# Kernel optimization log

Measured on AMD Instinct MI355X. Metric: run time of the kernel, lower is better.

The kernel has to match this reference:

```python
import jax, jax.numpy as jnp
import numpy as np

B, NQ, NK, D_IN, D_H = 2, 8192, 8192, 256, 256


def setup_inputs() -> dict:
    key = jax.random.key(0)
    ks = jax.random.split(key, 9)
    s = 1.0 / np.sqrt(D_IN)
    return {
        "q": jax.random.normal(ks[0], (B, NQ, D_IN), jnp.float32),
        "k": jax.random.normal(ks[1], (B, NK, D_IN), jnp.float32),
        "v": jax.random.normal(ks[2], (B, NK, D_IN), jnp.float32),
        "Wq": jax.random.uniform(ks[3], (D_IN, D_H), jnp.float32, -s, s),
        "bq": jax.random.uniform(ks[4], (D_H,), jnp.float32, -s, s),
        "Wk": jax.random.uniform(ks[5], (D_IN, D_H), jnp.float32, -s, s),
        "bk": jax.random.uniform(ks[6], (D_H,), jnp.float32, -s, s),
        "Wv": jax.random.uniform(ks[7], (D_IN, D_H), jnp.float32, -s, s),
        "bv": jax.random.uniform(ks[8], (D_H,), jnp.float32, -s, s),
        "chunk_size": 1024,
    }


def reference(q, k, v, Wq, bq, Wk, bk, Wv, bv, chunk_size):
    # Projections (nn.Linear: x @ W + b)
    q_emb = q @ Wq + bq            # [B, NQ, D_H]
    k_emb = k @ Wk + bk            # [B, NK, D_H]
    v_emb = v @ Wv + bv            # value_emb=True -> project v
    # NOTE: original applies NO 1/sqrt(d) scaling.
    # Query chunking in the original is a pure memory optimization;
    # softmax is over the full key axis, so full attention is identical math.
    scores = jnp.einsum("bqd,bkd->bqk", q_emb, k_emb)  # [B, NQ, NK]
    probs = jax.nn.softmax(scores, axis=-1)
    out = jnp.einsum("bqk,bkd->bqd", probs, v_emb)     # [B, NQ, D_H]
    return out
```

## Files before the change

### kernel.cpp

```cpp
#include <hip/hip_runtime.h>

#define B_   2
#define NQ_  8192
#define NK_  8192
#define DIN_ 256
#define DH_  256
#define M_   (B_ * NQ_)

typedef _Float16 f16x8 __attribute__((ext_vector_type(8)));
typedef unsigned short u16x8 __attribute__((ext_vector_type(8)));
typedef unsigned short u16x4 __attribute__((ext_vector_type(4)));
typedef unsigned int  u32x4 __attribute__((ext_vector_type(4)));
typedef float f32x16 __attribute__((ext_vector_type(16)));

__device__ __forceinline__ unsigned short f2h(float f) {
    _Float16 h = (_Float16)f;
    return __builtin_bit_cast(unsigned short, h);
}
__device__ __forceinline__ float h2f(unsigned short u) {
    return (float)__builtin_bit_cast(_Float16, u);
}

__global__ void wt_conv(const float* __restrict__ Wq, const float* __restrict__ Wk,
                        const float* __restrict__ Wv, unsigned short* __restrict__ wpack) {
    __shared__ float tile[64][65];
    const int mat = blockIdx.z;
    const int k0 = blockIdx.x * 64, n0 = blockIdx.y * 64;
    const float* W = (mat == 0) ? Wq : (mat == 1) ? Wk : Wv;
#pragma unroll
    for (int p = 0; p < 16; ++p) {
        const int idx = p * 256 + threadIdx.x;
        const int r = idx >> 6, c = idx & 63;
        tile[r][c] = W[(k0 + r) * 256 + n0 + c];
    }
    __syncthreads();
    unsigned short* wp = wpack + mat * 65536;
#pragma unroll
    for (int p = 0; p < 2; ++p) {
        const int e = p * 256 + threadIdx.x;
        const int kk8 = e >> 6;
        const int nn = e & 63;
        const int ks = (k0 >> 4) + (kk8 >> 1);
        const int lh = kk8 & 1;
        const int ng = (n0 >> 5) + (nn >> 5);
        const int l = (nn & 31) + 32 * lh;
        u16x8 val;
#pragma unroll
        for (int j = 0; j < 8; ++j) val[j] = f2h(tile[kk8 * 8 + j][nn]);
        *(u16x8*)(wp + ((size_t)(ks * 8 + ng) * 64 + l) * 8) = val;
    }
}

__global__ __launch_bounds__(256) void proj(
    const float* __restrict__ xq, const float* __restrict__ xk, const float* __restrict__ xv,
    const float* __restrict__ bq, const float* __restrict__ bk, const float* __restrict__ bv,
    const unsigned short* __restrict__ wpack,
    unsigned short* __restrict__ q_emb, unsigned short* __restrict__ k_emb,
    unsigned short* __restrict__ vpack) {
    __shared__ __align__(16) unsigned short xt[64 * 256];
    const int mat = blockIdx.y;
    const float* x    = (mat == 0) ? xq : (mat == 1) ? xk : xv;
    const float* bias = (mat == 0) ? bq : (mat == 1) ? bk : bv;
    const unsigned short* wp = wpack + mat * 65536;

    const int tid = threadIdx.x;
    const int l = tid & 63, wv = tid >> 6;
    const int pair = wv >> 1, h = wv & 1;
    const int lm = l & 31, lh = l >> 5;
    const int row0 = blockIdx.x * 64;

    {
        const float* xb = x + (size_t)row0 * 256;
#pragma unroll
        for (int p = 0; p < 8; ++p) {
            const int idx = p * 256 + tid;
            const int r = idx >> 5;
            const int c8 = idx & 31;
            const float4* ap = (const float4*)(xb + r * 256 + c8 * 8);
            float4 a0 = ap[0], a1 = ap[1];
            u16x8 au;
            au[0] = f2h(a0.x); au[1] = f2h(a0.y); au[2] = f2h(a0.z); au[3] = f2h(a0.w);
            au[4] = f2h(a1.x); au[5] = f2h(a1.y); au[6] = f2h(a1.z); au[7] = f2h(a1.w);
            *(u16x8*)(xt + r * 256 + (c8 ^ (r & 31)) * 8) = au;
        }
    }
    __syncthreads();

    f32x16 acc[4];
#pragma unroll
    for (int i = 0; i < 4; ++i)
#pragma unroll
        for (int j = 0; j < 16; ++j) acc[i][j] = 0.0f;

#pragma unroll
    for (int ks = 0; ks < 16; ++ks) {
        f16x8 af = *(const f16x8*)(xt + (pair * 32 + lm) * 256 +
                                   (((ks * 2 + lh) ^ lm) * 8));
#pragma unroll
        for (int nt = 0; nt < 4; ++nt) {
            f16x8 bfr = *(const f16x8*)(wp + ((size_t)(ks * 8 + h * 4 + nt) * 64 + l) * 8);
            acc[nt] = __builtin_amdgcn_mfma_f32_32x32x16_f16(af, bfr, acc[nt], 0, 0, 0);
        }
    }

    if (mat < 2) {
        unsigned short* emb = (mat == 0) ? q_emb : k_emb;
#pragma unroll
        for (int nt = 0; nt < 4; ++nt) {
            const int n = h * 128 + nt * 32 + lm;
            const float bsv = bias[n];
#pragma unroll
            for (int r = 0; r < 16; ++r) {
                const int rl = (r & 3) + 8 * (r >> 2) + 4 * lh;
                emb[(size_t)(row0 + pair * 32 + rl) * 256 + n] = f2h(acc[nt][r] + bsv);
            }
        }
    } else {
        const int batch = row0 >> 13;
        const int m0 = (row0 & 8191) + pair * 32;
        unsigned short* vp = vpack + (size_t)batch * (512 * 8 * 64 * 8);
        const int base_kt = m0 >> 4;
#pragma unroll
        for (int nt = 0; nt < 4; ++nt) {
            const int dg = h * 4 + nt;
            const int n = h * 128 + nt * 32 + lm;
            const float bsv = bias[n];
#pragma unroll
            for (int g = 0; g < 4; ++g) {
                u16x4 pk;
#pragma unroll
                for (int i = 0; i < 4; ++i) pk[i] = f2h(acc[nt][4 * g + i] + bsv);
                const int kt = base_kt + (g >> 1);
                const int lane = (g & 1) * 32 + lm;
                *(u16x4*)(vp + ((size_t)(kt * 8 + dg) * 64 + lane) * 8 + lh * 4) = pk;
            }
        }
    }
}

#define BN_ 128
#define NT_ (NK_ / BN_)
#define KB_BYTES 65536
#define PSTRIDE 272
#define PBYTES  (64 * PSTRIDE)
#define STAT_OFF (2 * KB_BYTES + PBYTES)
#define LDS_TOTAL (STAT_OFF + 2048)

__global__ __launch_bounds__(512, 2) void flash(
    const unsigned short* __restrict__ q_emb, const unsigned short* __restrict__ k_emb,
    const unsigned short* __restrict__ vpack, float* __restrict__ out) {
    __shared__ __align__(16) char lds_raw[LDS_TOTAL];
    char* pbuf = lds_raw + 2 * KB_BYTES;
    float* smax = (float*)(lds_raw + STAT_OFF);
    float* ssum = smax + 256;
    float* alph = ssum + 256;
    float* linvb = alph + 64;

    const int tid = threadIdx.x;
    const int l = tid & 63, wv = tid >> 6;
    const int kq = wv >> 1, pair = wv & 1;
    const int lm = l & 31, lh = l >> 5;

    const int bx = blockIdx.x;
    const int batch = bx >> 7;
    const int qb = (bx & 127) * 64;

    const unsigned short* kg = k_emb + (size_t)batch * NK_ * 256;
    const unsigned short* vp = vpack + (size_t)batch * (512 * 8 * 64 * 8);

    const int mrow = batch * NQ_ + qb + pair * 32 + lm;
    f16x8 qf[16];
#pragma unroll
    for (int ks = 0; ks < 16; ++ks)
        qf[ks] = *(const f16x8*)(q_emb + (size_t)mrow * 256 + ks * 16 + lh * 8);

    f32x16 oacc[2];
#pragma unroll
    for (int i = 0; i < 2; ++i)
#pragma unroll
        for (int j = 0; j < 16; ++j) oacc[i][j] = 0.0f;

    float mstat = -3.0e38f, lstat = 0.0f;

    const int rlane = l >> 5;
    const int gl = l & 31;
    auto stage_k = [&](int kb, char* kdst) {
#pragma unroll
        for (int p = 0; p < 8; ++p) {
            const int r0 = wv * 16 + 2 * p;
            const int r = r0 + rlane;
            const int gsw = gl ^ (r & 31);
            const unsigned short* src = kg + (size_t)(kb + r) * 256 + gsw * 8;
            __builtin_amdgcn_global_load_lds(
                (const __attribute__((address_space(1))) void*)src,
                (__attribute__((address_space(3))) void*)(kdst + r0 * 512),
                16, 0, 0);
        }
    };

    f16x8 vf[8];
    auto load_v = [&](int kb) {
        const size_t kt0 = (size_t)(kb >> 4);
#pragma unroll
        for (int ks2 = 0; ks2 < 8; ++ks2)
            vf[ks2] = *(const f16x8*)(vp + (((kt0 + ks2) * 8 + wv) * 64 + l) * 8);
    };

    stage_k(0, lds_raw);
    __syncthreads();

    const int prow = pair * 32 + lm;

    for (int t = 0; t < NT_; ++t) {
        const int kb = t * BN_;
        char* kcur = lds_raw + (t & 1) * KB_BYTES;
        if (t + 1 < NT_) stage_k(kb + BN_, lds_raw + ((t + 1) & 1) * KB_BYTES);
        load_v(kb);

        f32x16 s;
#pragma unroll
        for (int j = 0; j < 16; ++j) s[j] = 0.0f;
#pragma unroll
        for (int ks = 0; ks < 16; ++ks) {
            const int gsw = (2 * ks + lh) ^ lm;
            f16x8 kf = *(const f16x8*)(kcur + (kq * 32 + lm) * 512 + gsw * 16);
            s = __builtin_amdgcn_mfma_f32_32x32x16_f16(kf, qf[ks], s, 0, 0, 0);
        }

        float pm = s[0];
#pragma unroll
        for (int j = 1; j < 16; ++j) pm = fmaxf(pm, s[j]);
        pm = fmaxf(pm, __shfl_xor(pm, 32, 64));
        if (lh == 0) smax[prow * 4 + kq] = pm;
        __syncthreads();

        const float4 m4 = *(const float4*)&smax[prow * 4];
        const float gm = fmaxf(fmaxf(m4.x, m4.y), fmaxf(m4.z, m4.w));
        const float mn = fmaxf(mstat, gm);
        const float alpha = __expf(mstat - mn);
        mstat = mn;
        if (kq == 0 && lh == 0) alph[prow] = alpha;

        float psum = 0.0f;
#pragma unroll
        for (int g = 0; g < 4; ++g) {
            u16x4 pk;
#pragma unroll
            for (int j = 0; j < 4; ++j) {
                const unsigned short hh = f2h(__expf(s[g * 4 + j] - mn));
                pk[j] = hh;
                psum += h2f(hh);
            }
            *(u16x4*)(pbuf + prow * PSTRIDE + (kq * 32 + 8 * g + 4 * lh) * 2) = pk;
        }
        psum += __shfl_xor(psum, 32, 64);
        if (lh == 0) ssum[prow * 4 + kq] = psum;
        __syncthreads();

        const float4 s4 = *(const float4*)&ssum[prow * 4];
        lstat = lstat * alpha + (s4.x + s4.y) + (s4.z + s4.w);

        const float a0 = alph[lm];
        const float a1 = alph[lm + 32];
#pragma unroll
        for (int j = 0; j < 16; ++j) oacc[0][j] *= a0;
#pragma unroll
        for (int j = 0; j < 16; ++j) oacc[1][j] *= a1;

#pragma unroll
        for (int ks2 = 0; ks2 < 8; ++ks2) {
            const f16x8 vfr = vf[ks2];
            f16x8 pf0 = *(const f16x8*)(pbuf + lm * PSTRIDE + ks2 * 32 + lh * 16);
            f16x8 pf1 = *(const f16x8*)(pbuf + (lm + 32) * PSTRIDE + ks2 * 32 + lh * 16);
            oacc[0] = __builtin_amdgcn_mfma_f32_32x32x16_f16(vfr, pf0, oacc[0], 0, 0, 0);
            oacc[1] = __builtin_amdgcn_mfma_f32_32x32x16_f16(vfr, pf1, oacc[1], 0, 0, 0);
        }
    }

    if (kq == 0 && lh == 0) linvb[prow] = 1.0f / lstat;
    __syncthreads();
    const float linv0 = linvb[lm];
    const float linv1 = linvb[lm + 32];
#pragma unroll
    for (int qt = 0; qt < 2; ++qt) {
        const float lv = qt ? linv1 : linv0;
        float* orow = out + (size_t)(batch * NQ_ + qb + qt * 32 + lm) * 256 + wv * 32;
#pragma unroll
        for (int g = 0; g < 4; ++g) {
            float4 o4;
            o4.x = oacc[qt][4 * g + 0] * lv;
            o4.y = oacc[qt][4 * g + 1] * lv;
            o4.z = oacc[qt][4 * g + 2] * lv;
            o4.w = oacc[qt][4 * g + 3] * lv;
            *(float4*)(orow + 8 * g + 4 * lh) = o4;
        }
    }
}

extern "C" void kernel_launch(void* const* d_in, const int* in_sizes, int n_in,
                              void* d_out, int out_size, void* d_ws, size_t ws_size,
                              hipStream_t stream) {
    const float* q  = (const float*)d_in[0];
    const float* k  = (const float*)d_in[1];
    const float* v  = (const float*)d_in[2];
    const float* Wq = (const float*)d_in[3];
    const float* bq = (const float*)d_in[4];
    const float* Wk = (const float*)d_in[5];
    const float* bk = (const float*)d_in[6];
    const float* Wv = (const float*)d_in[7];
    const float* bv = (const float*)d_in[8];
    float* out = (float*)d_out;

    unsigned short* wpack   = (unsigned short*)d_ws;
    unsigned short* q_emb   = wpack + 3 * 65536;
    unsigned short* k_emb   = q_emb + (size_t)M_ * DH_;
    unsigned short* vpack   = k_emb + (size_t)M_ * DH_;

    wt_conv<<<dim3(4, 4, 3), 256, 0, stream>>>(Wq, Wk, Wv, wpack);
    proj<<<dim3(256, 3), 256, 0, stream>>>(q, k, v, bq, bk, bv, wpack, q_emb, k_emb, vpack);
    flash<<<256, 512, 0, stream>>>(q_emb, k_emb, vpack, out);
}
```

Before: 286.3 us.

## Split flash attention into specialized QK/softmax and PV warps with pipelined tiles

Restructures the flash kernel so that two waves compute QK^T scores and softmax while two other waves run the PV accumulation one tile behind, using double-buffered P, max and sum arrays in LDS. The key tile drops from 128 to 64, the query block from 64 to 32 rows, and the launch becomes 512 blocks of 256 threads. The goal is to overlap the softmax and QK MFMA work with the PV MFMA work and to let each PV wave reuse one P fragment across four output tiles. The cost is less MFMA parallelism per block, since only half the waves do each phase. Each K tile is also reloaded for only 32 queries, which doubles K traffic, and PV waves hold 64 accumulator registers plus 16 V fragments each.

```diff
diff --git a/kernel.cpp b/kernel.cpp
--- a/kernel.cpp
+++ b/kernel.cpp
@@ -138,49 +138,36 @@
     }
 }
 
-#define BN_ 128
-#define NT_ (NK_ / BN_)
-#define KB_BYTES 65536
-#define PSTRIDE 272
-#define PBYTES  (64 * PSTRIDE)
-#define STAT_OFF (2 * KB_BYTES + PBYTES)
-#define LDS_TOTAL (STAT_OFF + 2048)
-
-__global__ __launch_bounds__(512, 2) void flash(
+#define BN6_ 64
+#define NT6_ (NK_ / BN6_)
+#define KTILE_B 32768
+#define PST6 144
+#define PBUF_OFF (2 * KTILE_B)
+#define SMAX_OFF (PBUF_OFF + 2 * 32 * PST6)
+#define SSUM_OFF (SMAX_OFF + 512)
+#define LDS6_TOTAL (SSUM_OFF + 512)
+
+__global__ __launch_bounds__(256, 2) void flash(
     const unsigned short* __restrict__ q_emb, const unsigned short* __restrict__ k_emb,
     const unsigned short* __restrict__ vpack, float* __restrict__ out) {
-    __shared__ __align__(16) char lds_raw[LDS_TOTAL];
-    char* pbuf = lds_raw + 2 * KB_BYTES;
-    float* smax = (float*)(lds_raw + STAT_OFF);
-    float* ssum = smax + 256;
-    float* alph = ssum + 256;
-    float* linvb = alph + 64;
+    __shared__ __align__(16) char lds_raw[LDS6_TOTAL];
+    char* pb = lds_raw + PBUF_OFF;
+    float* smax = (float*)(lds_raw + SMAX_OFF);
+    float* ssum = (float*)(lds_raw + SSUM_OFF);
 
     const int tid = threadIdx.x;
     const int l = tid & 63, wv = tid >> 6;
-    const int kq = wv >> 1, pair = wv & 1;
     const int lm = l & 31, lh = l >> 5;
+    const bool is_s = (wv < 2);
+    const int kq = wv & 1;
+    const int pw = wv & 1;
 
     const int bx = blockIdx.x;
-    const int batch = bx >> 7;
-    const int qb = (bx & 127) * 64;
+    const int batch = bx >> 8;
+    const int qb = (bx & 255) * 32;
 
     const unsigned short* kg = k_emb + (size_t)batch * NK_ * 256;
     const unsigned short* vp = vpack + (size_t)batch * (512 * 8 * 64 * 8);
-
-    const int mrow = batch * NQ_ + qb + pair * 32 + lm;
-    f16x8 qf[16];
-#pragma unroll
-    for (int ks = 0; ks < 16; ++ks)
-        qf[ks] = *(const f16x8*)(q_emb + (size_t)mrow * 256 + ks * 16 + lh * 8);
-
-    f32x16 oacc[2];
-#pragma unroll
-    for (int i = 0; i < 2; ++i)
-#pragma unroll
-        for (int j = 0; j < 16; ++j) oacc[i][j] = 0.0f;
-
-    float mstat = -3.0e38f, lstat = 0.0f;
 
     const int rlane = l >> 5;
     const int gl = l & 31;
@@ -198,101 +185,147 @@
         }
     };
 
-    f16x8 vf[8];
-    auto load_v = [&](int kb) {
-        const size_t kt0 = (size_t)(kb >> 4);
-#pragma unroll
-        for (int ks2 = 0; ks2 < 8; ++ks2)
-            vf[ks2] = *(const f16x8*)(vp + (((kt0 + ks2) * 8 + wv) * 64 + l) * 8);
-    };
+    f16x8 qf[16];
+    float mstat_s = -3.0e38f;
+    f16x8 vf[16];
+    f32x16 oacc[4];
+    float mstat_p = -3.0e38f, lstat = 0.0f;
+
+    if (is_s) {
+        const int mrow = batch * NQ_ + qb + lm;
+#pragma unroll
+        for (int ks = 0; ks < 16; ++ks)
+            qf[ks] = *(const f16x8*)(q_emb + (size_t)mrow * 256 + ks * 16 + lh * 8);
+    } else {
+#pragma unroll
+        for (int i = 0; i < 4; ++i)
+#pragma unroll
+            for (int j = 0; j < 16; ++j) oacc[i][j] = 0.0f;
+    }
 
     stage_k(0, lds_raw);
     __syncthreads();
 
-    const int prow = pair * 32 + lm;
-
-    for (int t = 0; t < NT_; ++t) {
-        const int kb = t * BN_;
-        char* kcur = lds_raw + (t & 1) * KB_BYTES;
-        if (t + 1 < NT_) stage_k(kb + BN_, lds_raw + ((t + 1) & 1) * KB_BYTES);
-        load_v(kb);
+    for (int t = 0; t < NT6_; ++t) {
+        const int kb = t * BN6_;
+        if (t + 1 < NT6_) stage_k(kb + BN6_, lds_raw + ((t + 1) & 1) * KTILE_B);
 
         f32x16 s;
-#pragma unroll
-        for (int j = 0; j < 16; ++j) s[j] = 0.0f;
-#pragma unroll
-        for (int ks = 0; ks < 16; ++ks) {
-            const int gsw = (2 * ks + lh) ^ lm;
-            f16x8 kf = *(const f16x8*)(kcur + (kq * 32 + lm) * 512 + gsw * 16);
-            s = __builtin_amdgcn_mfma_f32_32x32x16_f16(kf, qf[ks], s, 0, 0, 0);
-        }
-
-        float pm = s[0];
-#pragma unroll
-        for (int j = 1; j < 16; ++j) pm = fmaxf(pm, s[j]);
-        pm = fmaxf(pm, __shfl_xor(pm, 32, 64));
-        if (lh == 0) smax[prow * 4 + kq] = pm;
+        if (is_s) {
+            char* kcur = lds_raw + (t & 1) * KTILE_B;
+#pragma unroll
+            for (int j = 0; j < 16; ++j) s[j] = 0.0f;
+#pragma unroll
+            for (int ks = 0; ks < 16; ++ks) {
+                const int gsw = (2 * ks + lh) ^ lm;
+                f16x8 kf = *(const f16x8*)(kcur + (kq * 32 + lm) * 512 + gsw * 16);
+                s = __builtin_amdgcn_mfma_f32_32x32x16_f16(kf, qf[ks], s, 0, 0, 0);
+            }
+            float pm = s[0];
+#pragma unroll
+            for (int j = 1; j < 16; ++j) pm = fmaxf(pm, s[j]);
+            pm = fmaxf(pm, __shfl_xor(pm, 32, 64));
+            if (lh == 0) smax[(t & 1) * 64 + lm * 2 + kq] = pm;
+        } else {
+            if (t > 0) {
+                const int pp = (t - 1) & 1;
+                const float m0 = smax[pp * 64 + lm * 2 + 0];
+                const float m1 = smax[pp * 64 + lm * 2 + 1];
+                const float gm = fmaxf(m0, m1);
+                const float mn = fmaxf(mstat_p, gm);
+                const float alpha = __expf(mstat_p - mn);
+                mstat_p = mn;
+                const float s0 = ssum[pp * 64 + lm * 2 + 0];
+                const float s1 = ssum[pp * 64 + lm * 2 + 1];
+                lstat = lstat * alpha + (s0 + s1);
+#pragma unroll
+                for (int dgi = 0; dgi < 4; ++dgi)
+#pragma unroll
+                    for (int j = 0; j < 16; ++j) oacc[dgi][j] *= alpha;
+                char* pbr = pb + pp * 32 * PST6;
+#pragma unroll
+                for (int ks2 = 0; ks2 < 4; ++ks2) {
+                    f16x8 pf = *(const f16x8*)(pbr + lm * PST6 + ks2 * 32 + lh * 16);
+#pragma unroll
+                    for (int dgi = 0; dgi < 4; ++dgi)
+                        oacc[dgi] = __builtin_amdgcn_mfma_f32_32x32x16_f16(
+                            vf[ks2 * 4 + dgi], pf, oacc[dgi], 0, 0, 0);
+                }
+            }
+            const size_t kt0 = (size_t)(kb >> 4);
+#pragma unroll
+            for (int ks2 = 0; ks2 < 4; ++ks2)
+#pragma unroll
+                for (int dgi = 0; dgi < 4; ++dgi)
+                    vf[ks2 * 4 + dgi] = *(const f16x8*)(
+                        vp + (((kt0 + ks2) * 8 + pw * 4 + dgi) * 64 + l) * 8);
+        }
         __syncthreads();
 
-        const float4 m4 = *(const float4*)&smax[prow * 4];
-        const float gm = fmaxf(fmaxf(m4.x, m4.y), fmaxf(m4.z, m4.w));
-        const float mn = fmaxf(mstat, gm);
-        const float alpha = __expf(mstat - mn);
-        mstat = mn;
-        if (kq == 0 && lh == 0) alph[prow] = alpha;
-
-        float psum = 0.0f;
-#pragma unroll
-        for (int g = 0; g < 4; ++g) {
-            u16x4 pk;
-#pragma unroll
-            for (int j = 0; j < 4; ++j) {
-                const unsigned short hh = f2h(__expf(s[g * 4 + j] - mn));
-                pk[j] = hh;
-                psum += h2f(hh);
-            }
-            *(u16x4*)(pbuf + prow * PSTRIDE + (kq * 32 + 8 * g + 4 * lh) * 2) = pk;
-        }
-        psum += __shfl_xor(psum, 32, 64);
-        if (lh == 0) ssum[prow * 4 + kq] = psum;
+        if (is_s) {
+            const float m0 = smax[(t & 1) * 64 + lm * 2 + 0];
+            const float m1 = smax[(t & 1) * 64 + lm * 2 + 1];
+            const float gm = fmaxf(m0, m1);
+            const float mn = fmaxf(mstat_s, gm);
+            mstat_s = mn;
+            char* pbw = pb + (t & 1) * 32 * PST6;
+            float psum = 0.0f;
+#pragma unroll
+            for (int g = 0; g < 4; ++g) {
+                u16x4 pk;
+#pragma unroll
+                for (int j = 0; j < 4; ++j) {
+                    const unsigned short hh = f2h(__expf(s[g * 4 + j] - mn));
+                    pk[j] = hh;
+                    psum += h2f(hh);
+                }
+                *(u16x4*)(pbw + lm * PST6 + kq * 64 + 16 * g + 8 * lh) = pk;
+            }
+            psum += __shfl_xor(psum, 32, 64);
+            if (lh == 0) ssum[(t & 1) * 64 + lm * 2 + kq] = psum;
+        }
         __syncthreads();
-
-        const float4 s4 = *(const float4*)&ssum[prow * 4];
-        lstat = lstat * alpha + (s4.x + s4.y) + (s4.z + s4.w);
-
-        const float a0 = alph[lm];
-        const float a1 = alph[lm + 32];
-#pragma unroll
-        for (int j = 0; j < 16; ++j) oacc[0][j] *= a0;
-#pragma unroll
-        for (int j = 0; j < 16; ++j) oacc[1][j] *= a1;
-
-#pragma unroll
-        for (int ks2 = 0; ks2 < 8; ++ks2) {
-            const f16x8 vfr = vf[ks2];
-            f16x8 pf0 = *(const f16x8*)(pbuf + lm * PSTRIDE + ks2 * 32 + lh * 16);
-            f16x8 pf1 = *(const f16x8*)(pbuf + (lm + 32) * PSTRIDE + ks2 * 32 + lh * 16);
-            oacc[0] = __builtin_amdgcn_mfma_f32_32x32x16_f16(vfr, pf0, oacc[0], 0, 0, 0);
-            oacc[1] = __builtin_amdgcn_mfma_f32_32x32x16_f16(vfr, pf1, oacc[1], 0, 0, 0);
-        }
-    }
-
-    if (kq == 0 && lh == 0) linvb[prow] = 1.0f / lstat;
-    __syncthreads();
-    const float linv0 = linvb[lm];
-    const float linv1 = linvb[lm + 32];
-#pragma unroll
-    for (int qt = 0; qt < 2; ++qt) {
-        const float lv = qt ? linv1 : linv0;
-        float* orow = out + (size_t)(batch * NQ_ + qb + qt * 32 + lm) * 256 + wv * 32;
-#pragma unroll
-        for (int g = 0; g < 4; ++g) {
-            float4 o4;
-            o4.x = oacc[qt][4 * g + 0] * lv;
-            o4.y = oacc[qt][4 * g + 1] * lv;
-            o4.z = oacc[qt][4 * g + 2] * lv;
-            o4.w = oacc[qt][4 * g + 3] * lv;
-            *(float4*)(orow + 8 * g + 4 * lh) = o4;
+    }
+
+    if (!is_s) {
+        const int pp = (NT6_ - 1) & 1;
+        const float m0 = smax[pp * 64 + lm * 2 + 0];
+        const float m1 = smax[pp * 64 + lm * 2 + 1];
+        const float gm = fmaxf(m0, m1);
+        const float mn = fmaxf(mstat_p, gm);
+        const float alpha = __expf(mstat_p - mn);
+        mstat_p = mn;
+        const float s0 = ssum[pp * 64 + lm * 2 + 0];
+        const float s1 = ssum[pp * 64 + lm * 2 + 1];
+        lstat = lstat * alpha + (s0 + s1);
+#pragma unroll
+        for (int dgi = 0; dgi < 4; ++dgi)
+#pragma unroll
+            for (int j = 0; j < 16; ++j) oacc[dgi][j] *= alpha;
+        char* pbr = pb + pp * 32 * PST6;
+#pragma unroll
+        for (int ks2 = 0; ks2 < 4; ++ks2) {
+            f16x8 pf = *(const f16x8*)(pbr + lm * PST6 + ks2 * 32 + lh * 16);
+#pragma unroll
+            for (int dgi = 0; dgi < 4; ++dgi)
+                oacc[dgi] = __builtin_amdgcn_mfma_f32_32x32x16_f16(
+                    vf[ks2 * 4 + dgi], pf, oacc[dgi], 0, 0, 0);
+        }
+
+        const float linv = 1.0f / lstat;
+        float* orow = out + (size_t)(batch * NQ_ + qb + lm) * 256;
+#pragma unroll
+        for (int dgi = 0; dgi < 4; ++dgi) {
+            const int d0 = (pw * 4 + dgi) * 32;
+#pragma unroll
+            for (int g = 0; g < 4; ++g) {
+                float4 o4;
+                o4.x = oacc[dgi][4 * g + 0] * linv;
+                o4.y = oacc[dgi][4 * g + 1] * linv;
+                o4.z = oacc[dgi][4 * g + 2] * linv;
+                o4.w = oacc[dgi][4 * g + 3] * linv;
+                *(float4*)(orow + d0 + 8 * g + 4 * lh) = o4;
+            }
         }
     }
 }
@@ -318,5 +351,5 @@
 
     wt_conv<<<dim3(4, 4, 3), 256, 0, stream>>>(Wq, Wk, Wv, wpack);
     proj<<<dim3(256, 3), 256, 0, stream>>>(q, k, v, bq, bk, bv, wpack, q_emb, k_emb, vpack);
-    flash<<<256, 512, 0, stream>>>(q_emb, k_emb, vpack, out);
-}
+    flash<<<512, 256, 0, stream>>>(q_emb, k_emb, vpack, out);
+}
```

New measurement: 608.4 us. 113% more time.
